# Kernel tuning notes

Hardware: AMD Instinct MI355X
Metric: run time of the kernel (lower is better)

Reference implementation:

```python
import jax, jax.numpy as jnp
import numpy as np

K = 20
EPS = 1e-5
SLOPE = 0.2


def lrelu(z):
    return jnp.where(z >= 0, z, SLOPE * z)


def knn(x, k):
    # x: [B, C, N] -> idx of k nearest neighbors [B, N, K]
    inner = -2.0 * jnp.einsum('bcn,bcm->bnm', x, x)
    xx = jnp.sum(x * x, axis=1)  # [B, N]
    pd = -xx[:, :, None] - inner - xx[:, None, :]  # negative squared distance
    _, idx = jax.lax.top_k(pd, k)
    return idx


def graph_feature(x, k):
    # x: [B, C, N] -> [B, 2C, N, K] = cat(neighbor - center, center)
    B, C, N = x.shape
    idx = knn(x, k)                                  # [B, N, K]
    x_bnc = jnp.transpose(x, (0, 2, 1))              # [B, N, C]
    nbr = x_bnc[jnp.arange(B)[:, None, None], idx]   # [B, N, K, C]
    ctr = x_bnc[:, :, None, :]                       # [B, N, 1, C]
    feat = jnp.concatenate(
        [nbr - ctr, jnp.broadcast_to(ctr, nbr.shape)], axis=-1)  # [B, N, K, 2C]
    return jnp.transpose(feat, (0, 3, 1, 2))         # [B, 2C, N, K]


def conv_bn_lrelu(x, w, g, b):
    # 1x1 conv (no bias) + BatchNorm2d (batch stats, train mode) + LeakyReLU(0.2)
    y = jnp.einsum('oc,bcnk->bonk', w, x)
    m = y.mean(axis=(0, 2, 3), keepdims=True)
    v = y.var(axis=(0, 2, 3), keepdims=True)
    y = (y - m) / jnp.sqrt(v + EPS) * g.reshape(1, -1, 1, 1) + b.reshape(1, -1, 1, 1)
    return lrelu(y)


def setup_inputs() -> dict:
    key = jax.random.key(0)
    ks = jax.random.split(key, 10)
    f32 = jnp.float32
    d = {
        'x': jax.random.normal(ks[0], (1, 3, 8, 4096), dtype=f32),
        'conv1_w': jax.random.normal(ks[1], (16, 6), dtype=f32) * 0.2,
        'bn1_g': jnp.ones((16,), f32), 'bn1_b': jnp.zeros((16,), f32),
        'conv2_w': jax.random.normal(ks[2], (32, 38), dtype=f32) * 0.1,
        'bn2_g': jnp.ones((32,), f32), 'bn2_b': jnp.zeros((32,), f32),
        'convd1_w': jax.random.normal(ks[3], (32, 32), dtype=f32) * 0.1,
        'bnd1_g': jnp.ones((32,), f32), 'bnd1_b': jnp.zeros((32,), f32),
        'convd2_w': jax.random.normal(ks[4], (32, 64), dtype=f32) * 0.1,
        'bnd2_g': jnp.ones((32,), f32), 'bnd2_b': jnp.zeros((32,), f32),
        'l1_w': jax.random.normal(ks[5], (64, 64), dtype=f32) * 0.1,
        'l1_b': jnp.zeros((64,), f32),
        'l2_w': jax.random.normal(ks[6], (32, 64), dtype=f32) * 0.1,
        'l2_b': jnp.zeros((32,), f32),
        'l3_w': jax.random.normal(ks[7], (11, 32), dtype=f32) * 0.1,
        'l3_b': jnp.zeros((11,), f32),
    }
    return d


def reference(x, conv1_w, bn1_g, bn1_b, conv2_w, bn2_g, bn2_b,
              convd1_w, bnd1_g, bnd1_b, convd2_w, bnd2_g, bnd2_b,
              l1_w, l1_b, l2_w, l2_b, l3_w, l3_b):
    x = jnp.transpose(x[0], (1, 0, 2))  # [B, 3, N]
    B, _, N = x.shape
    x1_gf = graph_feature(x, K)                                   # [B, 6, N, K]
    x1_max = conv_bn_lrelu(x1_gf, conv1_w, bn1_g, bn1_b).max(-1)  # [B, 16, N]
    gf16 = graph_feature(x1_max, K)                               # [B, 32, N, K]
    x2_gf = jnp.concatenate([x1_gf, gf16], axis=1)                # [B, 38, N, K]
    x2_max = conv_bn_lrelu(x2_gf, conv2_w, bn2_g, bn2_b).max(-1)  # [B, 32, N]
    xd1 = conv_bn_lrelu(gf16, convd1_w, bnd1_g, bnd1_b).max(-1)   # [B, 32, N]
    xd2 = conv_bn_lrelu(graph_feature(x2_max, K),
                        convd2_w, bnd2_g, bnd2_b).max(-1)          # [B, 32, N]
    h = jnp.concatenate([xd1, xd2], axis=1)                        # [B, 64, N]
    h = h.reshape(B, -1, 64).mean(axis=1)                          # raw view, as in torch
    h = lrelu(h @ l1_w.T + l1_b)
    h = lrelu(h @ l2_w.T + l2_b)
    return lrelu(h @ l3_w.T + l3_b)                                # [B, 11]
```

## Files before the change

kernel.cpp:

```cpp
#include <hip/hip_runtime.h>
#include <cstddef>

#define DI __device__ __forceinline__

constexpr int NB  = 8;
constexpr int NP  = 4096;
constexpr int KNN = 20;

DI float lrelu(float z) { return z >= 0.f ? z : 0.2f * z; }

__global__ void k_prep(const float* __restrict__ xin, float* __restrict__ xt,
                       float* __restrict__ xx) {
  int t = blockIdx.x * blockDim.x + threadIdx.x;
  int b = t >> 12, n = t & (NP - 1);
  float c0 = xin[(0 * NB + b) * NP + n];
  float c1 = xin[(1 * NB + b) * NP + n];
  float c2 = xin[(2 * NB + b) * NP + n];
  *reinterpret_cast<float4*>(xt + (size_t)t * 4) = make_float4(c0, c1, c2, 0.f);
  xx[t] = c0 * c0 + c1 * c1 + c2 * c2;
}

template<int C>
__global__ void k_xx(const float* __restrict__ X, float* __restrict__ xx) {
  int bn = blockIdx.x * blockDim.x + threadIdx.x;
  float s = 0.f;
#pragma unroll
  for (int c = 0; c < C; c += 4) {
    float4 a = *reinterpret_cast<const float4*>(X + (size_t)bn * C + c);
    s += a.x * a.x + a.y * a.y + a.z * a.z + a.w * a.w;
  }
  xx[bn] = s;
}

template<int C>
__global__ __launch_bounds__(256) void k_knn(const float* __restrict__ X,
                                             const float* __restrict__ xx,
                                             int* __restrict__ idxout) {
  constexpr int P  = 256;
  constexpr int CH = NP / P;
  constexpr int F4 = C / 4;
  __shared__ float4 lds[P * F4];

  int wv   = threadIdx.x >> 6;
  int lane = threadIdx.x & 63;
  int row  = blockIdx.x * 4 + wv;
  int b    = row >> 12;
  int n    = row & (NP - 1);
  const float* Xb  = X  + (size_t)b * NP * C;
  const float* xxb = xx + (size_t)b * NP;

  float q[C];
#pragma unroll
  for (int c = 0; c < C; c += 4) {
    float4 a = *reinterpret_cast<const float4*>(Xb + (size_t)n * C + c);
    q[c] = a.x; q[c + 1] = a.y; q[c + 2] = a.z; q[c + 3] = a.w;
  }
  float xxn = xxb[n];

  float v[64];
  float gv[4]; int gj[4];
#pragma unroll
  for (int g = 0; g < 4; ++g) { gv[g] = -3.0e38f; gj[g] = 0; }

#pragma unroll CH
  for (int ch = 0; ch < CH; ++ch) {
    __syncthreads();
    const float4* src = reinterpret_cast<const float4*>(Xb + (size_t)ch * P * C);
#pragma unroll
    for (int i = 0; i < F4; ++i) {
      int u = i * 256 + (int)threadIdx.x;
      int r = u >> 3, cc = u & 7;
      lds[r * 8 + (cc ^ (r & 7))] = src[u];
    }
    __syncthreads();
#pragma unroll
    for (int sl = 0; sl < 4; ++sl) {
      const int s = ch * 4 + sl;
      int p = sl * 64 + lane;
      float xxm = xxb[s * 64 + lane];
      float dot = 0.f;
#pragma unroll
      for (int cg = 0; cg < F4; ++cg) {
        int Fi = p * F4 + cg;
        int r = Fi >> 3, cc = Fi & 7;
        float4 a = lds[r * 8 + (cc ^ (r & 7))];
        dot = fmaf(q[cg * 4 + 0], a.x, dot);
        dot = fmaf(q[cg * 4 + 1], a.y, dot);
        dot = fmaf(q[cg * 4 + 2], a.z, dot);
        dot = fmaf(q[cg * 4 + 3], a.w, dot);
      }
      float val = 2.f * dot - xxm - xxn;
      v[s] = val;
      const int g = s >> 4;
      bool better = val > gv[g];
      gv[g] = better ? val : gv[g];
      gj[g] = better ? s   : gj[g];
    }
  }

  int gi[4];
#pragma unroll
  for (int g = 0; g < 4; ++g) gi[g] = (gj[g] << 6) | lane;

  int myidx = 0;
#pragma unroll 1
  for (int t = 0; t < KNN; ++t) {
    float bv = gv[0]; int bi = gi[0];
#pragma unroll
    for (int g = 1; g < 4; ++g) {
      bool bet = gv[g] > bv;
      bv = bet ? gv[g] : bv;
      bi = bet ? gi[g] : bi;
    }
#pragma unroll
    for (int off = 32; off >= 1; off >>= 1) {
      float ov = __shfl_xor(bv, off);
      int   oi = __shfl_xor(bi, off);
      bool bet = (ov > bv) || (ov == bv && oi < bi);
      bv = bet ? ov : bv;
      bi = bet ? oi : bi;
    }
    if (lane == t) myidx = bi;
    if (lane == (bi & 63)) {
      int jw = bi >> 6;
      int g  = jw >> 4;
#pragma unroll
      for (int G = 0; G < 4; ++G) {
        if (g == G) {
          float nv = -3.0e38f; int nj = 0;
#pragma unroll
          for (int jj = G * 16; jj < G * 16 + 16; ++jj) {
            v[jj] = (jj == jw) ? -3.4e38f : v[jj];
            bool bet = v[jj] > nv;
            nv = bet ? v[jj] : nv;
            nj = bet ? jj : nj;
          }
          gv[G] = nv;
          gi[G] = (nj << 6) | lane;
        }
      }
    }
  }
  if (lane < KNN) idxout[(size_t)row * KNN + lane] = myidx;
}

template<int CG>
DI void block_reduce_write(float (&s)[CG], float (&ss)[CG], float* red, float* out) {
#pragma unroll
  for (int o = 0; o < CG; ++o) {
#pragma unroll
    for (int off = 32; off >= 1; off >>= 1) {
      s[o]  += __shfl_xor(s[o],  off);
      ss[o] += __shfl_xor(ss[o], off);
    }
  }
  int lane = threadIdx.x & 63, wv = threadIdx.x >> 6;
  if (lane == 0) {
#pragma unroll
    for (int o = 0; o < CG; ++o) {
      red[wv * 2 * CG + o]      = s[o];
      red[wv * 2 * CG + CG + o] = ss[o];
    }
  }
  __syncthreads();
  if ((int)threadIdx.x < 2 * CG) {
    out[threadIdx.x] = red[0 * 2 * CG + threadIdx.x] + red[1 * 2 * CG + threadIdx.x] +
                       red[2 * 2 * CG + threadIdx.x] + red[3 * 2 * CG + threadIdx.x];
  }
}

template<int COUT, int CG, int OG, int KG>
__global__ void k_bnfin(const float* __restrict__ parts, const float* __restrict__ g,
                        const float* __restrict__ bb, float* __restrict__ bnp) {
  constexpr int G = 256 / COUT;
  __shared__ float red[512];
  int tid = threadIdx.x;
  int sub = tid / COUT, o = tid % COUT;
  int og = o / CG, oo = o % CG;
  float S = 0.f, SS = 0.f;
  for (int z = 0; z < KG; ++z)
    for (int x = sub; x < 128; x += G) {
      size_t p = ((size_t)(z * OG + og) * 128 + x) * (2 * CG);
      S  += parts[p + oo];
      SS += parts[p + CG + oo];
    }
  red[tid] = S; red[256 + tid] = SS;
  __syncthreads();
  if (tid < COUT) {
    S = 0.f; SS = 0.f;
#pragma unroll
    for (int gg = 0; gg < G; ++gg) { S += red[gg * COUT + tid]; SS += red[256 + gg * COUT + tid]; }
    const float cnt = (float)NB * NP * KNN;
    float m   = S / cnt;
    float var = SS / cnt - m * m;
    float sc  = g[tid] / sqrtf(var + 1e-5f);
    bnp[tid]        = sc;
    bnp[COUT + tid] = bb[tid] - m * sc;
  }
}

__global__ __launch_bounds__(256) void k_stats1(const float* __restrict__ xt,
    const int* __restrict__ idx1, const float* __restrict__ w, float* __restrict__ parts) {
  __shared__ float red[4 * 32];
  int bn = blockIdx.x * 256 + threadIdx.x;
  int b = bn >> 12;
  float4 ctr = *reinterpret_cast<const float4*>(xt + (size_t)bn * 4);
  float base[16], s[16], ss[16];
#pragma unroll
  for (int o = 0; o < 16; ++o) {
    const float* wo = w + o * 6;
    base[o] = (wo[3] - wo[0]) * ctr.x + (wo[4] - wo[1]) * ctr.y + (wo[5] - wo[2]) * ctr.z;
    s[o] = 0.f; ss[o] = 0.f;
  }
  const int* ip = idx1 + (size_t)bn * KNN + blockIdx.z * 10;
  for (int kk = 0; kk < 10; ++kk) {
    int m = ip[kk];
    float4 nb = *reinterpret_cast<const float4*>(xt + (size_t)(b * NP + m) * 4);
#pragma unroll
    for (int o = 0; o < 16; ++o) {
      const float* wo = w + o * 6;
      float y = fmaf(wo[0], nb.x, fmaf(wo[1], nb.y, fmaf(wo[2], nb.z, base[o])));
      s[o] += y; ss[o] = fmaf(y, y, ss[o]);
    }
  }
  size_t p = ((size_t)blockIdx.z * 128 + blockIdx.x) * 32;
  block_reduce_write<16>(s, ss, red, parts + p);
}

__global__ __launch_bounds__(256) void k_apply1(const float* __restrict__ xt,
    const int* __restrict__ idx1, const float* __restrict__ w, const float* __restrict__ bnp,
    float* __restrict__ x1m) {
  int bn = blockIdx.x * 256 + threadIdx.x;
  int og = blockIdx.y * 8;
  int b = bn >> 12;
  float4 ctr = *reinterpret_cast<const float4*>(xt + (size_t)bn * 4);
  float base[8], mx[8];
#pragma unroll
  for (int o = 0; o < 8; ++o) {
    const float* wo = w + (og + o) * 6;
    base[o] = (wo[3] - wo[0]) * ctr.x + (wo[4] - wo[1]) * ctr.y + (wo[5] - wo[2]) * ctr.z;
    mx[o] = -3.0e38f;
  }
  const int* ip = idx1 + (size_t)bn * KNN;
  for (int k = 0; k < KNN; ++k) {
    int m = ip[k];
    float4 nb = *reinterpret_cast<const float4*>(xt + (size_t)(b * NP + m) * 4);
#pragma unroll
    for (int o = 0; o < 8; ++o) {
      const float* wo = w + (og + o) * 6;
      float y = fmaf(wo[0], nb.x, fmaf(wo[1], nb.y, fmaf(wo[2], nb.z, base[o])));
      mx[o] = fmaxf(mx[o], lrelu(y * bnp[og + o] + bnp[16 + og + o]));
    }
  }
#pragma unroll
  for (int o = 0; o < 8; ++o) x1m[(size_t)bn * 16 + og + o] = mx[o];
}

__global__ __launch_bounds__(256) void k_stats2(const float* __restrict__ xt,
    const float* __restrict__ x1m, const int* __restrict__ idx1, const int* __restrict__ idx2,
    const float* __restrict__ w, float* __restrict__ parts) {
  __shared__ float red[4 * 16];
  int bn = blockIdx.x * 256 + threadIdx.x;
  int og = blockIdx.y * 8;
  int b = bn >> 12;
  float4 ctr3 = *reinterpret_cast<const float4*>(xt + (size_t)bn * 4);
  float base[8], s[8], ss[8];
#pragma unroll
  for (int o = 0; o < 8; ++o) {
    const float* wo = w + (og + o) * 38;
    base[o] = (wo[3] - wo[0]) * ctr3.x + (wo[4] - wo[1]) * ctr3.y + (wo[5] - wo[2]) * ctr3.z;
    s[o] = 0.f; ss[o] = 0.f;
  }
#pragma unroll
  for (int cg = 0; cg < 4; ++cg) {
    float4 a = *reinterpret_cast<const float4*>(x1m + (size_t)bn * 16 + cg * 4);
#pragma unroll
    for (int o = 0; o < 8; ++o) {
      const float* wo = w + (og + o) * 38;
      base[o] += (wo[22 + cg*4] - wo[6 + cg*4]) * a.x + (wo[23 + cg*4] - wo[7 + cg*4]) * a.y +
                 (wo[24 + cg*4] - wo[8 + cg*4]) * a.z + (wo[25 + cg*4] - wo[9 + cg*4]) * a.w;
    }
  }
  const int* i1 = idx1 + (size_t)bn * KNN + blockIdx.z * 10;
  const int* i2 = idx2 + (size_t)bn * KNN + blockIdx.z * 10;
  for (int kk = 0; kk < 10; ++kk) {
    int m1 = i1[kk], m2 = i2[kk];
    float4 nb3 = *reinterpret_cast<const float4*>(xt + (size_t)(b * NP + m1) * 4);
    float4 a0 = *reinterpret_cast<const float4*>(x1m + (size_t)(b * NP + m2) * 16 + 0);
    float4 a1 = *reinterpret_cast<const float4*>(x1m + (size_t)(b * NP + m2) * 16 + 4);
    float4 a2 = *reinterpret_cast<const float4*>(x1m + (size_t)(b * NP + m2) * 16 + 8);
    float4 a3 = *reinterpret_cast<const float4*>(x1m + (size_t)(b * NP + m2) * 16 + 12);
#pragma unroll
    for (int o = 0; o < 8; ++o) {
      const float* wo = w + (og + o) * 38;
      float y = base[o];
      y = fmaf(wo[0], nb3.x, y); y = fmaf(wo[1], nb3.y, y); y = fmaf(wo[2], nb3.z, y);
      y = fmaf(wo[6],  a0.x, y); y = fmaf(wo[7],  a0.y, y); y = fmaf(wo[8],  a0.z, y); y = fmaf(wo[9],  a0.w, y);
      y = fmaf(wo[10], a1.x, y); y = fmaf(wo[11], a1.y, y); y = fmaf(wo[12], a1.z, y); y = fmaf(wo[13], a1.w, y);
      y = fmaf(wo[14], a2.x, y); y = fmaf(wo[15], a2.y, y); y = fmaf(wo[16], a2.z, y); y = fmaf(wo[17], a2.w, y);
      y = fmaf(wo[18], a3.x, y); y = fmaf(wo[19], a3.y, y); y = fmaf(wo[20], a3.z, y); y = fmaf(wo[21], a3.w, y);
      s[o] += y; ss[o] = fmaf(y, y, ss[o]);
    }
  }
  size_t p = ((size_t)(blockIdx.z * 4 + blockIdx.y) * 128 + blockIdx.x) * 16;
  block_reduce_write<8>(s, ss, red, parts + p);
}

__global__ __launch_bounds__(256) void k_apply2(const float* __restrict__ xt,
    const float* __restrict__ x1m, const int* __restrict__ idx1, const int* __restrict__ idx2,
    const float* __restrict__ w, const float* __restrict__ bnp, float* __restrict__ x2m) {
  int bn = blockIdx.x * 256 + threadIdx.x;
  int og = blockIdx.y * 8;
  int b = bn >> 12;
  float4 ctr3 = *reinterpret_cast<const float4*>(xt + (size_t)bn * 4);
  float base[8], mx[8];
#pragma unroll
  for (int o = 0; o < 8; ++o) {
    const float* wo = w + (og + o) * 38;
    base[o] = (wo[3] - wo[0]) * ctr3.x + (wo[4] - wo[1]) * ctr3.y + (wo[5] - wo[2]) * ctr3.z;
    mx[o] = -3.0e38f;
  }
#pragma unroll
  for (int cg = 0; cg < 4; ++cg) {
    float4 a = *reinterpret_cast<const float4*>(x1m + (size_t)bn * 16 + cg * 4);
#pragma unroll
    for (int o = 0; o < 8; ++o) {
      const float* wo = w + (og + o) * 38;
      base[o] += (wo[22 + cg*4] - wo[6 + cg*4]) * a.x + (wo[23 + cg*4] - wo[7 + cg*4]) * a.y +
                 (wo[24 + cg*4] - wo[8 + cg*4]) * a.z + (wo[25 + cg*4] - wo[9 + cg*4]) * a.w;
    }
  }
  const int* i1 = idx1 + (size_t)bn * KNN;
  const int* i2 = idx2 + (size_t)bn * KNN;
  for (int k = 0; k < KNN; ++k) {
    int m1 = i1[k], m2 = i2[k];
    float4 nb3 = *reinterpret_cast<const float4*>(xt + (size_t)(b * NP + m1) * 4);
    float4 a0 = *reinterpret_cast<const float4*>(x1m + (size_t)(b * NP + m2) * 16 + 0);
    float4 a1 = *reinterpret_cast<const float4*>(x1m + (size_t)(b * NP + m2) * 16 + 4);
    float4 a2 = *reinterpret_cast<const float4*>(x1m + (size_t)(b * NP + m2) * 16 + 8);
    float4 a3 = *reinterpret_cast<const float4*>(x1m + (size_t)(b * NP + m2) * 16 + 12);
#pragma unroll
    for (int o = 0; o < 8; ++o) {
      const float* wo = w + (og + o) * 38;
      float y = base[o];
      y = fmaf(wo[0], nb3.x, y); y = fmaf(wo[1], nb3.y, y); y = fmaf(wo[2], nb3.z, y);
      y = fmaf(wo[6],  a0.x, y); y = fmaf(wo[7],  a0.y, y); y = fmaf(wo[8],  a0.z, y); y = fmaf(wo[9],  a0.w, y);
      y = fmaf(wo[10], a1.x, y); y = fmaf(wo[11], a1.y, y); y = fmaf(wo[12], a1.z, y); y = fmaf(wo[13], a1.w, y);
      y = fmaf(wo[14], a2.x, y); y = fmaf(wo[15], a2.y, y); y = fmaf(wo[16], a2.z, y); y = fmaf(wo[17], a2.w, y);
      y = fmaf(wo[18], a3.x, y); y = fmaf(wo[19], a3.y, y); y = fmaf(wo[20], a3.z, y); y = fmaf(wo[21], a3.w, y);
      mx[o] = fmaxf(mx[o], lrelu(y * bnp[og + o] + bnp[32 + og + o]));
    }
  }
#pragma unroll
  for (int o = 0; o < 8; ++o) x2m[(size_t)bn * 32 + og + o] = mx[o];
}

__global__ __launch_bounds__(256) void k_statsd1(const float* __restrict__ x1m,
    const int* __restrict__ idx2, const float* __restrict__ w, float* __restrict__ parts) {
  __shared__ float red[4 * 16];
  int bn = blockIdx.x * 256 + threadIdx.x;
  int og = blockIdx.y * 8;
  int b = bn >> 12;
  float base[8], s[8], ss[8];
#pragma unroll
  for (int o = 0; o < 8; ++o) { base[o] = 0.f; s[o] = 0.f; ss[o] = 0.f; }
#pragma unroll
  for (int cg = 0; cg < 4; ++cg) {
    float4 a = *reinterpret_cast<const float4*>(x1m + (size_t)bn * 16 + cg * 4);
#pragma unroll
    for (int o = 0; o < 8; ++o) {
      const float* wo = w + (og + o) * 32;
      base[o] += (wo[16 + cg*4] - wo[cg*4]) * a.x + (wo[17 + cg*4] - wo[1 + cg*4]) * a.y +
                 (wo[18 + cg*4] - wo[2 + cg*4]) * a.z + (wo[19 + cg*4] - wo[3 + cg*4]) * a.w;
    }
  }
  const int* i2 = idx2 + (size_t)bn * KNN + blockIdx.z * 10;
  for (int kk = 0; kk < 10; ++kk) {
    int m2 = i2[kk];
    float4 a0 = *reinterpret_cast<const float4*>(x1m + (size_t)(b * NP + m2) * 16 + 0);
    float4 a1 = *reinterpret_cast<const float4*>(x1m + (size_t)(b * NP + m2) * 16 + 4);
    float4 a2 = *reinterpret_cast<const float4*>(x1m + (size_t)(b * NP + m2) * 16 + 8);
    float4 a3 = *reinterpret_cast<const float4*>(x1m + (size_t)(b * NP + m2) * 16 + 12);
#pragma unroll
    for (int o = 0; o < 8; ++o) {
      const float* wo = w + (og + o) * 32;
      float y = base[o];
      y = fmaf(wo[0],  a0.x, y); y = fmaf(wo[1],  a0.y, y); y = fmaf(wo[2],  a0.z, y); y = fmaf(wo[3],  a0.w, y);
      y = fmaf(wo[4],  a1.x, y); y = fmaf(wo[5],  a1.y, y); y = fmaf(wo[6],  a1.z, y); y = fmaf(wo[7],  a1.w, y);
      y = fmaf(wo[8],  a2.x, y); y = fmaf(wo[9],  a2.y, y); y = fmaf(wo[10], a2.z, y); y = fmaf(wo[11], a2.w, y);
      y = fmaf(wo[12], a3.x, y); y = fmaf(wo[13], a3.y, y); y = fmaf(wo[14], a3.z, y); y = fmaf(wo[15], a3.w, y);
      s[o] += y; ss[o] = fmaf(y, y, ss[o]);
    }
  }
  size_t p = ((size_t)(blockIdx.z * 4 + blockIdx.y) * 128 + blockIdx.x) * 16;
  block_reduce_write<8>(s, ss, red, parts + p);
}

__global__ __launch_bounds__(256) void k_applyd1(const float* __restrict__ x1m,
    const int* __restrict__ idx2, const float* __restrict__ w, const float* __restrict__ bnp,
    float* __restrict__ xd1) {
  int bn = blockIdx.x * 256 + threadIdx.x;
  int og = blockIdx.y * 8;
  int b = bn >> 12;
  float base[8], mx[8];
#pragma unroll
  for (int o = 0; o < 8; ++o) { base[o] = 0.f; mx[o] = -3.0e38f; }
#pragma unroll
  for (int cg = 0; cg < 4; ++cg) {
    float4 a = *reinterpret_cast<const float4*>(x1m + (size_t)bn * 16 + cg * 4);
#pragma unroll
    for (int o = 0; o < 8; ++o) {
      const float* wo = w + (og + o) * 32;
      base[o] += (wo[16 + cg*4] - wo[cg*4]) * a.x + (wo[17 + cg*4] - wo[1 + cg*4]) * a.y +
                 (wo[18 + cg*4] - wo[2 + cg*4]) * a.z + (wo[19 + cg*4] - wo[3 + cg*4]) * a.w;
    }
  }
  const int* i2 = idx2 + (size_t)bn * KNN;
  for (int k = 0; k < KNN; ++k) {
    int m2 = i2[k];
    float4 a0 = *reinterpret_cast<const float4*>(x1m + (size_t)(b * NP + m2) * 16 + 0);
    float4 a1 = *reinterpret_cast<const float4*>(x1m + (size_t)(b * NP + m2) * 16 + 4);
    float4 a2 = *reinterpret_cast<const float4*>(x1m + (size_t)(b * NP + m2) * 16 + 8);
    float4 a3 = *reinterpret_cast<const float4*>(x1m + (size_t)(b * NP + m2) * 16 + 12);
#pragma unroll
    for (int o = 0; o < 8; ++o) {
      const float* wo = w + (og + o) * 32;
      float y = base[o];
      y = fmaf(wo[0],  a0.x, y); y = fmaf(wo[1],  a0.y, y); y = fmaf(wo[2],  a0.z, y); y = fmaf(wo[3],  a0.w, y);
      y = fmaf(wo[4],  a1.x, y); y = fmaf(wo[5],  a1.y, y); y = fmaf(wo[6],  a1.z, y); y = fmaf(wo[7],  a1.w, y);
      y = fmaf(wo[8],  a2.x, y); y = fmaf(wo[9],  a2.y, y); y = fmaf(wo[10], a2.z, y); y = fmaf(wo[11], a2.w, y);
      y = fmaf(wo[12], a3.x, y); y = fmaf(wo[13], a3.y, y); y = fmaf(wo[14], a3.z, y); y = fmaf(wo[15], a3.w, y);
      mx[o] = fmaxf(mx[o], lrelu(y * bnp[og + o] + bnp[32 + og + o]));
    }
  }
#pragma unroll
  for (int o = 0; o < 8; ++o) xd1[(size_t)bn * 32 + og + o] = mx[o];
}

__global__ __launch_bounds__(256) void k_statsd2(const float* __restrict__ x2m,
    const int* __restrict__ idx3, const float* __restrict__ w, float* __restrict__ parts) {
  __shared__ float red[4 * 16];
  int bn = blockIdx.x * 256 + threadIdx.x;
  int og = blockIdx.y * 8;
  int b = bn >> 12;
  float base[8], s[8], ss[8];
#pragma unroll
  for (int o = 0; o < 8; ++o) { base[o] = 0.f; s[o] = 0.f; ss[o] = 0.f; }
#pragma unroll
  for (int cg = 0; cg < 8; ++cg) {
    float4 a = *reinterpret_cast<const float4*>(x2m + (size_t)bn * 32 + cg * 4);
#pragma unroll
    for (int o = 0; o < 8; ++o) {
      const float* wo = w + (og + o) * 64;
      base[o] += (wo[32 + cg*4] - wo[cg*4]) * a.x + (wo[33 + cg*4] - wo[1 + cg*4]) * a.y +
                 (wo[34 + cg*4] - wo[2 + cg*4]) * a.z + (wo[35 + cg*4] - wo[3 + cg*4]) * a.w;
    }
  }
  const int* i3 = idx3 + (size_t)bn * KNN + blockIdx.z * 10;
  for (int kk = 0; kk < 10; ++kk) {
    int m3 = i3[kk];
    const float* np = x2m + (size_t)(b * NP + m3) * 32;
    float4 a0 = *reinterpret_cast<const float4*>(np + 0);
    float4 a1 = *reinterpret_cast<const float4*>(np + 4);
    float4 a2 = *reinterpret_cast<const float4*>(np + 8);
    float4 a3 = *reinterpret_cast<const float4*>(np + 12);
    float4 a4 = *reinterpret_cast<const float4*>(np + 16);
    float4 a5 = *reinterpret_cast<const float4*>(np + 20);
    float4 a6 = *reinterpret_cast<const float4*>(np + 24);
    float4 a7 = *reinterpret_cast<const float4*>(np + 28);
#pragma unroll
    for (int o = 0; o < 8; ++o) {
      const float* wo = w + (og + o) * 64;
      float y = base[o];
      y = fmaf(wo[0],  a0.x, y); y = fmaf(wo[1],  a0.y, y); y = fmaf(wo[2],  a0.z, y); y = fmaf(wo[3],  a0.w, y);
      y = fmaf(wo[4],  a1.x, y); y = fmaf(wo[5],  a1.y, y); y = fmaf(wo[6],  a1.z, y); y = fmaf(wo[7],  a1.w, y);
      y = fmaf(wo[8],  a2.x, y); y = fmaf(wo[9],  a2.y, y); y = fmaf(wo[10], a2.z, y); y = fmaf(wo[11], a2.w, y);
      y = fmaf(wo[12], a3.x, y); y = fmaf(wo[13], a3.y, y); y = fmaf(wo[14], a3.z, y); y = fmaf(wo[15], a3.w, y);
      y = fmaf(wo[16], a4.x, y); y = fmaf(wo[17], a4.y, y); y = fmaf(wo[18], a4.z, y); y = fmaf(wo[19], a4.w, y);
      y = fmaf(wo[20], a5.x, y); y = fmaf(wo[21], a5.y, y); y = fmaf(wo[22], a5.z, y); y = fmaf(wo[23], a5.w, y);
      y = fmaf(wo[24], a6.x, y); y = fmaf(wo[25], a6.y, y); y = fmaf(wo[26], a6.z, y); y = fmaf(wo[27], a6.w, y);
      y = fmaf(wo[28], a7.x, y); y = fmaf(wo[29], a7.y, y); y = fmaf(wo[30], a7.z, y); y = fmaf(wo[31], a7.w, y);
      s[o] += y; ss[o] = fmaf(y, y, ss[o]);
    }
  }
  size_t p = ((size_t)(blockIdx.z * 4 + blockIdx.y) * 128 + blockIdx.x) * 16;
  block_reduce_write<8>(s, ss, red, parts + p);
}

__global__ __launch_bounds__(256) void k_applyd2(const float* __restrict__ x2m,
    const int* __restrict__ idx3, const float* __restrict__ w, const float* __restrict__ bnp,
    float* __restrict__ xd2) {
  int bn = blockIdx.x * 256 + threadIdx.x;
  int og = blockIdx.y * 8;
  int b = bn >> 12;
  float base[8], mx[8];
#pragma unroll
  for (int o = 0; o < 8; ++o) { base[o] = 0.f; mx[o] = -3.0e38f; }
#pragma unroll
  for (int cg = 0; cg < 8; ++cg) {
    float4 a = *reinterpret_cast<const float4*>(x2m + (size_t)bn * 32 + cg * 4);
#pragma unroll
    for (int o = 0; o < 8; ++o) {
      const float* wo = w + (og + o) * 64;
      base[o] += (wo[32 + cg*4] - wo[cg*4]) * a.x + (wo[33 + cg*4] - wo[1 + cg*4]) * a.y +
                 (wo[34 + cg*4] - wo[2 + cg*4]) * a.z + (wo[35 + cg*4] - wo[3 + cg*4]) * a.w;
    }
  }
  const int* i3 = idx3 + (size_t)bn * KNN;
  for (int k = 0; k < KNN; ++k) {
    int m3 = i3[k];
    const float* np = x2m + (size_t)(b * NP + m3) * 32;
    float4 a0 = *reinterpret_cast<const float4*>(np + 0);
    float4 a1 = *reinterpret_cast<const float4*>(np + 4);
    float4 a2 = *reinterpret_cast<const float4*>(np + 8);
    float4 a3 = *reinterpret_cast<const float4*>(np + 12);
    float4 a4 = *reinterpret_cast<const float4*>(np + 16);
    float4 a5 = *reinterpret_cast<const float4*>(np + 20);
    float4 a6 = *reinterpret_cast<const float4*>(np + 24);
    float4 a7 = *reinterpret_cast<const float4*>(np + 28);
#pragma unroll
    for (int o = 0; o < 8; ++o) {
      const float* wo = w + (og + o) * 64;
      float y = base[o];
      y = fmaf(wo[0],  a0.x, y); y = fmaf(wo[1],  a0.y, y); y = fmaf(wo[2],  a0.z, y); y = fmaf(wo[3],  a0.w, y);
      y = fmaf(wo[4],  a1.x, y); y = fmaf(wo[5],  a1.y, y); y = fmaf(wo[6],  a1.z, y); y = fmaf(wo[7],  a1.w, y);
      y = fmaf(wo[8],  a2.x, y); y = fmaf(wo[9],  a2.y, y); y = fmaf(wo[10], a2.z, y); y = fmaf(wo[11], a2.w, y);
      y = fmaf(wo[12], a3.x, y); y = fmaf(wo[13], a3.y, y); y = fmaf(wo[14], a3.z, y); y = fmaf(wo[15], a3.w, y);
      y = fmaf(wo[16], a4.x, y); y = fmaf(wo[17], a4.y, y); y = fmaf(wo[18], a4.z, y); y = fmaf(wo[19], a4.w, y);
      y = fmaf(wo[20], a5.x, y); y = fmaf(wo[21], a5.y, y); y = fmaf(wo[22], a5.z, y); y = fmaf(wo[23], a5.w, y);
      y = fmaf(wo[24], a6.x, y); y = fmaf(wo[25], a6.y, y); y = fmaf(wo[26], a6.z, y); y = fmaf(wo[27], a6.w, y);
      y = fmaf(wo[28], a7.x, y); y = fmaf(wo[29], a7.y, y); y = fmaf(wo[30], a7.z, y); y = fmaf(wo[31], a7.w, y);
      mx[o] = fmaxf(mx[o], lrelu(y * bnp[og + o] + bnp[32 + og + o]));
    }
  }
#pragma unroll
  for (int o = 0; o < 8; ++o) xd2[(size_t)bn * 32 + og + o] = mx[o];
}

__global__ void k_mean(const float* __restrict__ xd1, const float* __restrict__ xd2,
                       float* __restrict__ hm) {
  int b = blockIdx.x >> 6, j = blockIdx.x & 63;
  int tt = threadIdx.x;
  const float* p1 = xd1 + ((size_t)(b * NP) + tt * 64 + j) * 32;
  const float* p2 = xd2 + ((size_t)(b * NP) + tt * 64 + j) * 32;
  float s = 0.f;
#pragma unroll
  for (int c = 0; c < 32; c += 4) {
    float4 a = *reinterpret_cast<const float4*>(p1 + c);
    s += a.x + a.y + a.z + a.w;
  }
#pragma unroll
  for (int c = 0; c < 32; c += 4) {
    float4 a = *reinterpret_cast<const float4*>(p2 + c);
    s += a.x + a.y + a.z + a.w;
  }
#pragma unroll
  for (int off = 32; off >= 1; off >>= 1) s += __shfl_xor(s, off);
  if (tt == 0) hm[blockIdx.x] = s * (1.f / 4096.f);
}

__global__ void k_mlp(const float* __restrict__ hm,
                      const float* __restrict__ w1, const float* __restrict__ b1,
                      const float* __restrict__ w2, const float* __restrict__ b2,
                      const float* __restrict__ w3, const float* __restrict__ b3,
                      float* __restrict__ out) {
  __shared__ float h0[512], h1[512], h2[256];
  int t = threadIdx.x;
  h0[t] = hm[t];
  __syncthreads();
  {
    int b = t >> 6, o = t & 63;
    float a = b1[o];
    for (int j = 0; j < 64; ++j) a += h0[b * 64 + j] * w1[o * 64 + j];
    h1[t] = lrelu(a);
  }
  __syncthreads();
  if (t < 256) {
    int b = t >> 5, o = t & 31;
    float a = b2[o];
    for (int j = 0; j < 64; ++j) a += h1[b * 64 + j] * w2[o * 64 + j];
    h2[t] = lrelu(a);
  }
  __syncthreads();
  if (t < 88) {
    int b = t / 11, o = t % 11;
    float a = b3[o];
    for (int j = 0; j < 32; ++j) a += h2[b * 32 + j] * w3[o * 32 + j];
    out[t] = lrelu(a);
  }
}

extern "C" void kernel_launch(void* const* d_in, const int* in_sizes, int n_in,
                              void* d_out, int out_size, void* d_ws, size_t ws_size,
                              hipStream_t stream) {
  const float* xin = (const float*)d_in[0];
  const float* w1  = (const float*)d_in[1];
  const float* g1  = (const float*)d_in[2];
  const float* bb1 = (const float*)d_in[3];
  const float* w2  = (const float*)d_in[4];
  const float* g2  = (const float*)d_in[5];
  const float* bb2 = (const float*)d_in[6];
  const float* wd1 = (const float*)d_in[7];
  const float* gd1 = (const float*)d_in[8];
  const float* bbd1= (const float*)d_in[9];
  const float* wd2 = (const float*)d_in[10];
  const float* gd2 = (const float*)d_in[11];
  const float* bbd2= (const float*)d_in[12];
  const float* l1w = (const float*)d_in[13];
  const float* l1b = (const float*)d_in[14];
  const float* l2w = (const float*)d_in[15];
  const float* l2b = (const float*)d_in[16];
  const float* l3w = (const float*)d_in[17];
  const float* l3b = (const float*)d_in[18];
  float* out = (float*)d_out;

  float* W = (float*)d_ws;
  float* xt    = W;
  float* xx1   = W + 131072;
  float* xx2   = W + 163840;
  float* xx3   = W + 196608;
  float* x1m   = W + 229376;
  float* x2m   = W + 753664;
  float* xd1   = W + 1802240;
  float* xd2   = W + 2850816;
  float* hmean = W + 3899392;
  float* bnp1  = W + 3899904;
  float* bnp2  = W + 3899968;
  float* bnpd1 = W + 3900032;
  float* bnpd2 = W + 3900096;
  float* parts = W + 3900160;
  int* idx1 = (int*)(W + 3932928);
  int* idx2 = idx1 + 655360;
  int* idx3 = idx2 + 655360;

  k_prep<<<128, 256, 0, stream>>>(xin, xt, xx1);
  k_knn<4><<<8192, 256, 0, stream>>>(xt, xx1, idx1);

  k_stats1<<<dim3(128, 1, 2), 256, 0, stream>>>(xt, idx1, w1, parts);
  k_bnfin<16, 16, 1, 2><<<1, 256, 0, stream>>>(parts, g1, bb1, bnp1);
  k_apply1<<<dim3(128, 2), 256, 0, stream>>>(xt, idx1, w1, bnp1, x1m);
  k_xx<16><<<128, 256, 0, stream>>>(x1m, xx2);
  k_knn<16><<<8192, 256, 0, stream>>>(x1m, xx2, idx2);

  k_stats2<<<dim3(128, 4, 2), 256, 0, stream>>>(xt, x1m, idx1, idx2, w2, parts);
  k_bnfin<32, 8, 4, 2><<<1, 256, 0, stream>>>(parts, g2, bb2, bnp2);
  k_apply2<<<dim3(128, 4), 256, 0, stream>>>(xt, x1m, idx1, idx2, w2, bnp2, x2m);
  k_xx<32><<<128, 256, 0, stream>>>(x2m, xx3);

  k_statsd1<<<dim3(128, 4, 2), 256, 0, stream>>>(x1m, idx2, wd1, parts);
  k_bnfin<32, 8, 4, 2><<<1, 256, 0, stream>>>(parts, gd1, bbd1, bnpd1);
  k_applyd1<<<dim3(128, 4), 256, 0, stream>>>(x1m, idx2, wd1, bnpd1, xd1);

  k_knn<32><<<8192, 256, 0, stream>>>(x2m, xx3, idx3);
  k_statsd2<<<dim3(128, 4, 2), 256, 0, stream>>>(x2m, idx3, wd2, parts);
  k_bnfin<32, 8, 4, 2><<<1, 256, 0, stream>>>(parts, gd2, bbd2, bnpd2);
  k_applyd2<<<dim3(128, 4), 256, 0, stream>>>(x2m, idx3, wd2, bnpd2, xd2);

  k_mean<<<512, 64, 0, stream>>>(xd1, xd2, hmean);
  k_mlp<<<1, 512, 0, stream>>>(hmean, l1w, l1b, l2w, l2b, l3w, l3b, out);
}
```

Before: 1.946 ms.

## Split kNN candidates across waves, 4 query rows per wave, then rank-merge partial top-k

The kNN kernel used to give each wave one query row and stream every candidate through LDS behind block-wide barriers. Now each wave scores one quarter of the candidates (1024) against all four query rows of the block. It reads candidate features straight from global memory in 16-channel passes and keeps 4x16 partial dot products in registers. Each wave selects a per-row top-20 over its own slice, and the four partial lists are merged through shared memory by rank counting. This removes the LDS staging and its barriers and shortens the per-row selection scan, at the cost of higher register pressure and uncached global candidate loads.

```diff
diff --git a/kernel.cpp b/kernel.cpp
--- a/kernel.cpp
+++ b/kernel.cpp
@@ -36,112 +36,135 @@
 __global__ __launch_bounds__(256) void k_knn(const float* __restrict__ X,
                                              const float* __restrict__ xx,
                                              int* __restrict__ idxout) {
-  constexpr int P  = 256;
-  constexpr int CH = NP / P;
-  constexpr int F4 = C / 4;
-  __shared__ float4 lds[P * F4];
-
-  int wv   = threadIdx.x >> 6;
-  int lane = threadIdx.x & 63;
-  int row  = blockIdx.x * 4 + wv;
-  int b    = row >> 12;
-  int n    = row & (NP - 1);
+  constexpr int NPASS = (C + 15) / 16;
+  __shared__ float mv[4][4][20];
+  __shared__ int   mi[4][4][20];
+
+  int wv = threadIdx.x >> 6;
+  int ln = threadIdx.x & 63;
+  int row0 = blockIdx.x * 4;
+  int b  = row0 >> 12;
+  int n0 = row0 & (NP - 1);
   const float* Xb  = X  + (size_t)b * NP * C;
   const float* xxb = xx + (size_t)b * NP;
 
-  float q[C];
-#pragma unroll
-  for (int c = 0; c < C; c += 4) {
-    float4 a = *reinterpret_cast<const float4*>(Xb + (size_t)n * C + c);
-    q[c] = a.x; q[c + 1] = a.y; q[c + 2] = a.z; q[c + 3] = a.w;
-  }
-  float xxn = xxb[n];
-
-  float v[64];
-  float gv[4]; int gj[4];
-#pragma unroll
-  for (int g = 0; g < 4; ++g) { gv[g] = -3.0e38f; gj[g] = 0; }
-
-#pragma unroll CH
-  for (int ch = 0; ch < CH; ++ch) {
-    __syncthreads();
-    const float4* src = reinterpret_cast<const float4*>(Xb + (size_t)ch * P * C);
-#pragma unroll
-    for (int i = 0; i < F4; ++i) {
-      int u = i * 256 + (int)threadIdx.x;
-      int r = u >> 3, cc = u & 7;
-      lds[r * 8 + (cc ^ (r & 7))] = src[u];
-    }
-    __syncthreads();
-#pragma unroll
-    for (int sl = 0; sl < 4; ++sl) {
-      const int s = ch * 4 + sl;
-      int p = sl * 64 + lane;
-      float xxm = xxb[s * 64 + lane];
-      float dot = 0.f;
-#pragma unroll
-      for (int cg = 0; cg < F4; ++cg) {
-        int Fi = p * F4 + cg;
-        int r = Fi >> 3, cc = Fi & 7;
-        float4 a = lds[r * 8 + (cc ^ (r & 7))];
-        dot = fmaf(q[cg * 4 + 0], a.x, dot);
-        dot = fmaf(q[cg * 4 + 1], a.y, dot);
-        dot = fmaf(q[cg * 4 + 2], a.z, dot);
-        dot = fmaf(q[cg * 4 + 3], a.w, dot);
+  float xxn[4];
+#pragma unroll
+  for (int r = 0; r < 4; ++r) xxn[r] = xxb[n0 + r];
+
+  float v[4][16];
+#pragma unroll
+  for (int r = 0; r < 4; ++r)
+#pragma unroll
+    for (int cc = 0; cc < 16; ++cc) v[r][cc] = 0.f;
+
+  float q[64];
+#pragma unroll
+  for (int pass = 0; pass < NPASS; ++pass) {
+    const int c0 = pass * 16;
+    const int CW = (C - c0 >= 16) ? 16 : (C - c0);
+#pragma unroll
+    for (int r = 0; r < 4; ++r)
+#pragma unroll
+      for (int j = 0; j < CW; j += 4) {
+        float4 a = *reinterpret_cast<const float4*>(&Xb[(size_t)(n0 + r) * C + c0 + j]);
+        q[r * 16 + j] = a.x; q[r * 16 + j + 1] = a.y;
+        q[r * 16 + j + 2] = a.z; q[r * 16 + j + 3] = a.w;
       }
-      float val = 2.f * dot - xxm - xxn;
-      v[s] = val;
-      const int g = s >> 4;
-      bool better = val > gv[g];
-      gv[g] = better ? val : gv[g];
-      gj[g] = better ? s   : gj[g];
-    }
-  }
-
-  int gi[4];
-#pragma unroll
-  for (int g = 0; g < 4; ++g) gi[g] = (gj[g] << 6) | lane;
-
-  int myidx = 0;
+#pragma unroll 2
+    for (int cc = 0; cc < 16; ++cc) {
+      int cand = wv * 1024 + cc * 64 + ln;
+      float4 cr[4];
+#pragma unroll
+      for (int cb = 0; cb * 4 < CW; ++cb)
+        cr[cb] = *reinterpret_cast<const float4*>(&Xb[(size_t)cand * C + c0 + cb * 4]);
+#pragma unroll
+      for (int r = 0; r < 4; ++r) {
+        float dot = v[r][cc];
+#pragma unroll
+        for (int cb = 0; cb * 4 < CW; ++cb) {
+          dot = fmaf(q[r * 16 + cb * 4 + 0], cr[cb].x, dot);
+          dot = fmaf(q[r * 16 + cb * 4 + 1], cr[cb].y, dot);
+          dot = fmaf(q[r * 16 + cb * 4 + 2], cr[cb].z, dot);
+          dot = fmaf(q[r * 16 + cb * 4 + 3], cr[cb].w, dot);
+        }
+        v[r][cc] = dot;
+      }
+    }
+  }
+
+  float gv[4][2]; int gj[4][2];
+#pragma unroll
+  for (int r = 0; r < 4; ++r) { gv[r][0] = -3.0e38f; gv[r][1] = -3.0e38f; gj[r][0] = 0; gj[r][1] = 0; }
+#pragma unroll 2
+  for (int cc = 0; cc < 16; ++cc) {
+    int cand = wv * 1024 + cc * 64 + ln;
+    float xxm = xxb[cand];
+#pragma unroll
+    for (int r = 0; r < 4; ++r) {
+      float val = fmaf(2.f, v[r][cc], -xxn[r]) - xxm;
+      v[r][cc] = val;
+      const int g = cc >> 3;
+      bool bet = val > gv[r][g];
+      gv[r][g] = bet ? val : gv[r][g];
+      gj[r][g] = bet ? cand : gj[r][g];
+    }
+  }
+
+#pragma unroll
+  for (int r = 0; r < 4; ++r) {
+    float myv = -3.0e38f; int myi = 0;
 #pragma unroll 1
-  for (int t = 0; t < KNN; ++t) {
-    float bv = gv[0]; int bi = gi[0];
-#pragma unroll
-    for (int g = 1; g < 4; ++g) {
-      bool bet = gv[g] > bv;
-      bv = bet ? gv[g] : bv;
-      bi = bet ? gi[g] : bi;
-    }
-#pragma unroll
-    for (int off = 32; off >= 1; off >>= 1) {
-      float ov = __shfl_xor(bv, off);
-      int   oi = __shfl_xor(bi, off);
-      bool bet = (ov > bv) || (ov == bv && oi < bi);
-      bv = bet ? ov : bv;
-      bi = bet ? oi : bi;
-    }
-    if (lane == t) myidx = bi;
-    if (lane == (bi & 63)) {
-      int jw = bi >> 6;
-      int g  = jw >> 4;
-#pragma unroll
-      for (int G = 0; G < 4; ++G) {
-        if (g == G) {
+    for (int t = 0; t < KNN; ++t) {
+      bool b1 = gv[r][1] > gv[r][0];
+      float bv = b1 ? gv[r][1] : gv[r][0];
+      int   bi = b1 ? gj[r][1] : gj[r][0];
+#pragma unroll
+      for (int off = 32; off >= 1; off >>= 1) {
+        float ov = __shfl_xor(bv, off);
+        int   oi = __shfl_xor(bi, off);
+        bool bet = (ov > bv) || (ov == bv && oi < bi);
+        bv = bet ? ov : bv;
+        bi = bet ? oi : bi;
+      }
+      if (ln == t) { myv = bv; myi = bi; }
+      if (ln == (bi & 63)) {
+        int ccw = (bi >> 6) & 15;
+        int g = ccw >> 3;
+#pragma unroll
+        for (int G = 0; G < 2; ++G) if (G == g) {
           float nv = -3.0e38f; int nj = 0;
 #pragma unroll
-          for (int jj = G * 16; jj < G * 16 + 16; ++jj) {
-            v[jj] = (jj == jw) ? -3.4e38f : v[jj];
-            bool bet = v[jj] > nv;
-            nv = bet ? v[jj] : nv;
-            nj = bet ? jj : nj;
+          for (int j = G * 8; j < G * 8 + 8; ++j) {
+            v[r][j] = (j == ccw) ? -3.4e38f : v[r][j];
+            bool bet = v[r][j] > nv;
+            nv = bet ? v[r][j] : nv;
+            nj = bet ? j : nj;
           }
-          gv[G] = nv;
-          gi[G] = (nj << 6) | lane;
+          gv[r][G] = nv;
+          gj[r][G] = wv * 1024 + nj * 64 + ln;
         }
       }
     }
-  }
-  if (lane < KNN) idxout[(size_t)row * KNN + lane] = myidx;
+    if (ln < KNN) { mv[r][wv][ln] = myv; mi[r][wv][ln] = myi; }
+  }
+  __syncthreads();
+
+  const float* fv = &mv[wv][0][0];
+  const int*   fi = &mi[wv][0][0];
+  float e0v = fv[ln];  int e0i = fi[ln];
+  float e1v = (ln < 16) ? fv[64 + ln] : -3.4e38f;
+  int   e1i = (ln < 16) ? fi[64 + ln] : -1;
+  int r0 = 0, r1 = 0;
+#pragma unroll 4
+  for (int j = 0; j < 80; ++j) {
+    float jv = fv[j]; int ji = fi[j];
+    r0 += ((jv > e0v) || (jv == e0v && ji < e0i)) ? 1 : 0;
+    r1 += ((jv > e1v) || (jv == e1v && ji < e1i)) ? 1 : 0;
+  }
+  int row = row0 + wv;
+  if (r0 < KNN) idxout[(size_t)row * KNN + r0] = e0i;
+  if (ln < 16 && r1 < KNN) idxout[(size_t)row * KNN + r1] = e1i;
 }
 
 template<int CG>
```

Result: slower. 2.960 ms (+52.1%).
